# Performance work log

Hardware: AMD Instinct MI355X
Metric: run time of the kernel (lower is better)

## Reference

```python
import jax, jax.numpy as jnp
import numpy as np

N_A = 50000
N_B = 50000
E = 800000
C_IN = 128
C_OUT = 128


def _lstm_cell_seq1(x, W_ih, b):
    # PyTorch LSTM with seq_len=1 and zero initial state: h = o*tanh(i*g)
    # gate order in weight_ih: [i, f, g, o]; f-gate is unused since c0 = 0.
    gates = x @ W_ih.T + b  # [N, 4H]
    i, f, g, o = jnp.split(gates, 4, axis=-1)
    c = jax.nn.sigmoid(i) * jnp.tanh(g)
    return jax.nn.sigmoid(o) * jnp.tanh(c)


def _conv(x_src, x_dst, edge_index, W_ih, b_lstm, W_lin, b_lin):
    # LSTM message depends only on src features -> compute per node, gather per edge.
    msg = _lstm_cell_seq1(x_src, W_ih, b_lstm)          # [N_src, C_OUT]
    src, dst = edge_index[0], edge_index[1]
    aggr = jax.ops.segment_sum(msg[src], dst, num_segments=x_dst.shape[0])  # [N_dst, C_OUT]
    h = jnp.concatenate([x_dst, aggr], axis=-1)          # [N_dst, C_IN + C_OUT]
    return jax.nn.relu(h @ W_lin.T + b_lin)              # dropout = identity (eval mode)


def setup_inputs() -> dict:
    key = jax.random.key(0)
    ks = jax.random.split(key, 12)
    s = 0.05
    return {
        "x_a": jax.random.normal(ks[0], (N_A, C_IN), jnp.float32),
        "x_b": jax.random.normal(ks[1], (N_B, C_IN), jnp.float32),
        "edge_ab": jax.random.randint(ks[2], (2, E), 0, 50000, jnp.int64 if jax.config.jax_enable_x64 else jnp.int32),
        "edge_ba": jax.random.randint(ks[3], (2, E), 0, 50000, jnp.int64 if jax.config.jax_enable_x64 else jnp.int32),
        "W_ih_ab": jax.random.normal(ks[4], (4 * C_OUT, C_IN), jnp.float32) * s,
        "b_ab": jax.random.normal(ks[5], (4 * C_OUT,), jnp.float32) * s,
        "W_lin_ab": jax.random.normal(ks[6], (C_OUT, C_IN + C_OUT), jnp.float32) * s,
        "b_lin_ab": jax.random.normal(ks[7], (C_OUT,), jnp.float32) * s,
        "W_ih_ba": jax.random.normal(ks[8], (4 * C_OUT, C_IN), jnp.float32) * s,
        "b_ba": jax.random.normal(ks[9], (4 * C_OUT,), jnp.float32) * s,
        "W_lin_ba": jax.random.normal(ks[10], (C_OUT, C_IN + C_OUT), jnp.float32) * s,
        "b_lin_ba": jax.random.normal(ks[11], (C_OUT,), jnp.float32) * s,
    }


def reference(x_a, x_b, edge_ab, edge_ba,
              W_ih_ab, b_ab, W_lin_ab, b_lin_ab,
              W_ih_ba, b_ba, W_lin_ba, b_lin_ba):
    # a_to_b relation updates type_b nodes; b_to_a updates type_a nodes.
    out_b = _conv(x_a, x_b, edge_ab, W_ih_ab, b_ab, W_lin_ab, b_lin_ab)
    out_a = _conv(x_b, x_a, edge_ba, W_ih_ba, b_ba, W_lin_ba, b_lin_ba)
    # stack (same shapes) => [2, N, C_OUT]: index 0 = new x_a, index 1 = new x_b
    return jnp.stack([out_a, out_b], axis=0)
```

## Files before the change

kernel.cpp:

```cpp
#include <hip/hip_runtime.h>
#include <cstdint>
#include <cstddef>

#define CCH 128
#define TK 4096
#define FCAP 5120
#define SLOT 5120
#define MAXBKT 512
#define XPAD 136
#define APAD 264

typedef __attribute__((ext_vector_type(8))) short short8;
typedef __attribute__((ext_vector_type(4))) float floatx4;

__device__ __forceinline__ unsigned short f2bf(float f) {
    unsigned u = __builtin_bit_cast(unsigned, f);
    u += 0x7fffu + ((u >> 16) & 1u);
    return (unsigned short)(u >> 16);
}
__device__ __forceinline__ float bf2f(unsigned short h) {
    unsigned u = ((unsigned)h) << 16;
    return __builtin_bit_cast(float, u);
}
__device__ __forceinline__ float sigmoidf_(float x) { return 1.0f / (1.0f + __expf(-x)); }
__device__ __forceinline__ float tanh_fast(float x) {
    x = fminf(fmaxf(x, -10.0f), 10.0f);
    float e = __expf(2.0f * x);
    return (e - 1.0f) / (e + 1.0f);
}

__global__ __launch_bounds__(256) void prep_weights_kernel(
    const float* __restrict__ Wih0, const float* __restrict__ Wih1,
    const float* __restrict__ Wlin0, const float* __restrict__ Wlin1,
    unsigned short* __restrict__ frag_ih, unsigned short* __restrict__ frag_lin)
{
    int t = blockIdx.x * 256 + threadIdx.x;
    if (t < 12288) {
        int l  = t & 63;
        int kc = (t >> 6) & 3;
        int ct = (t >> 8) & 7;
        int g  = (t >> 11) % 3;
        int rel = t / 6144;
        int gb = (g == 0) ? 0 : (g == 1 ? 256 : 384);
        const float* W = rel ? Wih1 : Wih0;
        int n  = gb + ct * 16 + (l & 15);
        int kb = kc * 32 + (l >> 4) * 8;
        unsigned short* o = frag_ih + (size_t)t * 8;
#pragma unroll
        for (int j = 0; j < 8; j++) o[j] = f2bf(W[(size_t)n * CCH + kb + j]);
    } else {
        int t2 = t - 12288;
        if (t2 >= 8192) return;
        int l  = t2 & 63;
        int kc = (t2 >> 6) & 7;
        int ct = (t2 >> 9) & 7;
        int rel = t2 >> 12;
        const float* W = rel ? Wlin1 : Wlin0;
        int n  = ct * 16 + (l & 15);
        int kb = kc * 32 + (l >> 4) * 8;
        unsigned short* o = frag_lin + (size_t)t2 * 8;
#pragma unroll
        for (int j = 0; j < 8; j++) o[j] = f2bf(W[(size_t)n * 256 + kb + j]);
    }
}

__global__ __launch_bounds__(256) void lstm_hist_kernel(
    const float* __restrict__ x0, const float* __restrict__ x1,
    const unsigned short* __restrict__ wfrag,
    const float* __restrict__ b0, const float* __restrict__ b1,
    unsigned short* __restrict__ msg0, unsigned short* __restrict__ msg1,
    int N0, int N1, int nblk0,
    const int* __restrict__ dstE0, const int* __restrict__ dstE1,
    int* __restrict__ H, int E0, int E1, int nbkt0, int NBKT, int nT)
{
    __shared__ unsigned short xs[32 * XPAD];
    __shared__ int h[MAXBKT];
    const int tid = threadIdx.x;

    if (blockIdx.x < nT) {
        for (int i = tid; i < NBKT; i += 256) h[i] = 0;
        __syncthreads();
        const long long Etot = (long long)E0 + E1;
        const long long base = (long long)blockIdx.x * TK;
        for (int i = tid; i < TK; i += 256) {
            long long e = base + i;
            if (e >= Etot) break;
            int g;
            if (e < E0) g = dstE0[e] >> 8;
            else        g = nbkt0 + (dstE1[e - E0] >> 8);
            atomicAdd(&h[g], 1);
        }
        __syncthreads();
        int* row = H + (size_t)blockIdx.x * NBKT;
        for (int i = tid; i < NBKT; i += 256) row[i] = h[i];
        return;
    }

    const int lb = blockIdx.x - nT;
    const int rel = (lb >= nblk0);
    const int nb = (rel ? (lb - nblk0) : lb) * 32;
    const float* x = rel ? x1 : x0;
    const float* bias = rel ? b1 : b0;
    unsigned short* msg = rel ? msg1 : msg0;
    const int N = rel ? N1 : N0;
    const unsigned short* wf = wfrag + (size_t)rel * 6144 * 8;

    {
        int r = tid >> 3;
        int c0 = (tid & 7) * 16;
        int n = nb + r;
        unsigned short* dstp = xs + r * XPAD + c0;
        if (n < N) {
            const float4* srcp = (const float4*)(x + (size_t)n * CCH + c0);
#pragma unroll
            for (int qq = 0; qq < 4; qq++) {
                float4 v = srcp[qq];
                unsigned u0 = (unsigned)f2bf(v.x) | ((unsigned)f2bf(v.y) << 16);
                unsigned u1 = (unsigned)f2bf(v.z) | ((unsigned)f2bf(v.w) << 16);
                *(uint2*)(dstp + qq * 4) = make_uint2(u0, u1);
            }
        } else {
#pragma unroll
            for (int qq = 0; qq < 4; qq++) *(uint2*)(dstp + qq * 4) = make_uint2(0u, 0u);
        }
    }
    __syncthreads();

    const int w = tid >> 6;
    const int l = tid & 63;
    const int ctb2 = w * 2;
    const int q = l >> 4;
    const int m16 = l & 15;

    floatx4 acc[3][2][2];
#pragma unroll
    for (int g = 0; g < 3; g++)
#pragma unroll
        for (int c = 0; c < 2; c++)
#pragma unroll
            for (int mt = 0; mt < 2; mt++) acc[g][c][mt] = (floatx4){0.f, 0.f, 0.f, 0.f};

    const unsigned short* arow0 = xs + m16 * XPAD + q * 8;
    const unsigned short* arow1 = xs + (16 + m16) * XPAD + q * 8;
#pragma unroll
    for (int kc = 0; kc < 4; kc++) {
        short8 af0 = *(const short8*)(arow0 + kc * 32);
        short8 af1 = *(const short8*)(arow1 + kc * 32);
#pragma unroll
        for (int g = 0; g < 3; g++)
#pragma unroll
            for (int c = 0; c < 2; c++) {
                const unsigned short* bp = wf + ((((size_t)g * 8 + (ctb2 + c)) * 4 + kc) * 64 + l) * 8;
                short8 bv = *(const short8*)bp;
                acc[g][c][0] = __builtin_amdgcn_mfma_f32_16x16x32_bf16(af0, bv, acc[g][c][0], 0, 0, 0);
                acc[g][c][1] = __builtin_amdgcn_mfma_f32_16x16x32_bf16(af1, bv, acc[g][c][1], 0, 0, 0);
            }
    }

    __syncthreads();
#pragma unroll
    for (int c = 0; c < 2; c++) {
        const int col = (ctb2 + c) * 16 + m16;
        const float bi = bias[col], bg = bias[256 + col], bo = bias[384 + col];
#pragma unroll
        for (int mt = 0; mt < 2; mt++)
#pragma unroll
            for (int r = 0; r < 4; r++) {
                const int nl = mt * 16 + q * 4 + r;
                float iv = sigmoidf_(acc[0][c][mt][r] + bi);
                float gv = tanh_fast(acc[1][c][mt][r] + bg);
                float ov = sigmoidf_(acc[2][c][mt][r] + bo);
                xs[nl * XPAD + col] = f2bf(ov * tanh_fast(iv * gv));
            }
    }
    __syncthreads();
    {
        int r = tid >> 3;
        int c0 = (tid & 7) * 16;
        int n = nb + r;
        if (n < N) {
            const unsigned short* srow = xs + r * XPAD + c0;
            uint4 v0 = *(const uint4*)(srow);
            uint4 v1 = *(const uint4*)(srow + 8);
            unsigned short* drow = msg + (size_t)n * CCH + c0;
            *(uint4*)(drow) = v0;
            *(uint4*)(drow + 8) = v1;
        }
    }
}

__global__ __launch_bounds__(256) void colscan_kernel(
    int* __restrict__ H, int* __restrict__ btot, int nT, int NBKT)
{
    __shared__ int s[256];
    __shared__ int carry;
    const int g = blockIdx.x;
    const int tid = threadIdx.x;
    if (tid == 0) carry = 0;
    __syncthreads();
    for (int base = 0; base < nT; base += 256) {
        int b = base + tid;
        int v = (b < nT) ? H[(size_t)b * NBKT + g] : 0;
        s[tid] = v;
        __syncthreads();
#pragma unroll
        for (int off = 1; off < 256; off <<= 1) {
            int t = (tid >= off) ? s[tid - off] : 0;
            __syncthreads();
            s[tid] += t;
            __syncthreads();
        }
        if (b < nT) H[(size_t)b * NBKT + g] = s[tid] - v + carry;
        __syncthreads();
        if (tid == 255) carry += s[255];
        __syncthreads();
    }
    if (tid == 0) btot[g] = carry;
}

__global__ __launch_bounds__(256) void tile_scatter_kernel(
    const int* __restrict__ src0, const int* __restrict__ dst0,
    const int* __restrict__ src1, const int* __restrict__ dst1,
    const int* __restrict__ H,
    unsigned* __restrict__ packed, int E0, int E1, int nbkt0, int NBKT)
{
    __shared__ int cur[MAXBKT];
    const int tid = threadIdx.x;
    const int* row = H + (size_t)blockIdx.x * NBKT;
    for (int i = tid; i < NBKT; i += 256) cur[i] = i * SLOT + row[i];
    __syncthreads();
    const long long Etot = (long long)E0 + E1;
    const long long base = (long long)blockIdx.x * TK;
    for (int i = tid; i < TK; i += 256) {
        long long e = base + i;
        if (e >= Etot) break;
        int s, g, k;
        if (e < E0) { int d = dst0[e]; s = src0[e]; g = d >> 8; k = d & 255; }
        else { long long ee = e - E0; int d = dst1[ee]; s = src1[ee]; g = nbkt0 + (d >> 8); k = d & 255; }
        int pos = atomicAdd(&cur[g], 1);
        packed[pos] = ((unsigned)k << 24) | (unsigned)s;
    }
}

__global__ __launch_bounds__(256) void fine_sort_kernel(
    unsigned* __restrict__ packed, const int* __restrict__ btot,
    int* __restrict__ offs0, int* __restrict__ deg0,
    int* __restrict__ offs1, int* __restrict__ deg1,
    int N0, int N1, int nbkt0)
{
    __shared__ unsigned pin[FCAP];
    __shared__ int sout[FCAP];
    __shared__ int hist[256], scn[256], cur[256];
    const int g = blockIdx.x;
    const int tid = threadIdx.x;
    const int base = g * SLOT;
    const int cnt = min(btot[g], FCAP);

    for (int i = tid; i < cnt; i += 256) pin[i] = packed[base + i];
    hist[tid] = 0;
    __syncthreads();
    for (int i = tid; i < cnt; i += 256) atomicAdd(&hist[pin[i] >> 24], 1);
    __syncthreads();
    int v = hist[tid];
    scn[tid] = v;
    __syncthreads();
#pragma unroll
    for (int off = 1; off < 256; off <<= 1) {
        int t = (tid >= off) ? scn[tid - off] : 0;
        __syncthreads();
        scn[tid] += t;
        __syncthreads();
    }
    int excl = scn[tid] - v;
    cur[tid] = excl;
    {
        const int rel = (g >= nbkt0);
        const int lb = rel ? g - nbkt0 : g;
        const int n = lb * 256 + tid;
        const int N = rel ? N1 : N0;
        if (n < N) {
            if (rel) { offs1[n] = base + excl; deg1[n] = v; }
            else     { offs0[n] = base + excl; deg0[n] = v; }
        }
    }
    __syncthreads();
    for (int i = tid; i < cnt; i += 256) {
        unsigned p = pin[i];
        int pos = atomicAdd(&cur[p >> 24], 1);
        sout[pos] = (int)(p & 0x00FFFFFFu);
    }
    __syncthreads();
    int* op = (int*)packed;
    for (int i = tid; i < cnt; i += 256) op[base + i] = sout[i];
}

__global__ __launch_bounds__(512) void gather_linear_kernel(
    const float* __restrict__ xd0, const float* __restrict__ xd1,
    const unsigned short* __restrict__ msg0, const unsigned short* __restrict__ msg1,
    const int* __restrict__ csr,
    const int* __restrict__ offs0, const int* __restrict__ offs1,
    const int* __restrict__ deg0, const int* __restrict__ deg1,
    const unsigned short* __restrict__ wfrag,
    const float* __restrict__ bl0, const float* __restrict__ bl1,
    float* __restrict__ out0, float* __restrict__ out1,
    int P0, int P1, int N0, int N1)
{
    __shared__ unsigned short s[32 * APAD];
    const int tid = threadIdx.x;
    const int grp = blockIdx.x >> 3;
    const int sub = blockIdx.x & 7;
    const int rel = (sub >> 2) & 1;
    const int lb = grp * 4 + (sub & 3);
    const int P = rel ? P1 : P0;
    if (lb >= P) return;
    const int nb = lb * 32;
    const float* xd = rel ? xd1 : xd0;
    const unsigned short* msg = rel ? msg1 : msg0;
    const int* offs = rel ? offs1 : offs0;
    const int* deg = rel ? deg1 : deg0;
    const float* bl = rel ? bl1 : bl0;
    float* outp = rel ? out1 : out0;
    const int N = rel ? N1 : N0;
    const unsigned short* wf = wfrag + (size_t)rel * 4096 * 8;

    {
        int r = tid >> 4;
        int c0 = (tid & 15) * 8;
        int n = nb + r;
        unsigned short* drow = s + r * APAD + c0;
        if (n < N) {
            const float4* srcp = (const float4*)(xd + (size_t)n * CCH + c0);
            float4 v0 = srcp[0], v1 = srcp[1];
            uint4 u;
            u.x = (unsigned)f2bf(v0.x) | ((unsigned)f2bf(v0.y) << 16);
            u.y = (unsigned)f2bf(v0.z) | ((unsigned)f2bf(v0.w) << 16);
            u.z = (unsigned)f2bf(v1.x) | ((unsigned)f2bf(v1.y) << 16);
            u.w = (unsigned)f2bf(v1.z) | ((unsigned)f2bf(v1.w) << 16);
            *(uint4*)drow = u;
        } else {
            *(uint4*)drow = make_uint4(0u, 0u, 0u, 0u);
        }
    }
    {
        const int w = tid >> 6;
        const int l = tid & 63;
        const int g = l >> 4;
        const int c = l & 15;
        const int nloc = w * 4 + g;
        const int n = nb + nloc;
        float a0 = 0.f, a1 = 0.f, a2 = 0.f, a3 = 0.f;
        float a4 = 0.f, a5 = 0.f, a6 = 0.f, a7 = 0.f;
        if (n < N) {
            const int start = offs[n];
            const int cnt = deg[n];
            const int* ce = csr + start;
            const unsigned short* mb = msg + c * 8;
#define ACC8(U) { \
            a0 += bf2f((unsigned short)(U.x)); a1 += bf2f((unsigned short)((U.x) >> 16)); \
            a2 += bf2f((unsigned short)(U.y)); a3 += bf2f((unsigned short)((U.y) >> 16)); \
            a4 += bf2f((unsigned short)(U.z)); a5 += bf2f((unsigned short)((U.z) >> 16)); \
            a6 += bf2f((unsigned short)(U.w)); a7 += bf2f((unsigned short)((U.w) >> 16)); }
            int j = 0;
            for (; j + 4 <= cnt; j += 4) {
                int s0 = ce[j], s1 = ce[j + 1], s2 = ce[j + 2], s3 = ce[j + 3];
                uint4 u0 = *(const uint4*)(mb + (size_t)s0 * CCH);
                uint4 u1 = *(const uint4*)(mb + (size_t)s1 * CCH);
                uint4 u2 = *(const uint4*)(mb + (size_t)s2 * CCH);
                uint4 u3 = *(const uint4*)(mb + (size_t)s3 * CCH);
                ACC8(u0); ACC8(u1); ACC8(u2); ACC8(u3);
            }
            for (; j < cnt; j++) {
                uint4 u0 = *(const uint4*)(mb + (size_t)ce[j] * CCH);
                ACC8(u0);
            }
#undef ACC8
        }
        uint4 o;
        o.x = (unsigned)f2bf(a0) | ((unsigned)f2bf(a1) << 16);
        o.y = (unsigned)f2bf(a2) | ((unsigned)f2bf(a3) << 16);
        o.z = (unsigned)f2bf(a4) | ((unsigned)f2bf(a5) << 16);
        o.w = (unsigned)f2bf(a6) | ((unsigned)f2bf(a7) << 16);
        *(uint4*)(s + nloc * APAD + CCH + c * 8) = o;
    }
    __syncthreads();

    const int w = tid >> 6;
    const int l = tid & 63;
    const int q = l >> 4;
    const int m16 = l & 15;

    floatx4 acc[2];
    acc[0] = (floatx4){0.f, 0.f, 0.f, 0.f};
    acc[1] = (floatx4){0.f, 0.f, 0.f, 0.f};

    const unsigned short* arow0 = s + m16 * APAD + q * 8;
    const unsigned short* arow1 = s + (16 + m16) * APAD + q * 8;
#pragma unroll
    for (int kc = 0; kc < 8; kc++) {
        short8 af0 = *(const short8*)(arow0 + kc * 32);
        short8 af1 = *(const short8*)(arow1 + kc * 32);
        const unsigned short* bp = wf + ((((size_t)w) * 8 + kc) * 64 + l) * 8;
        short8 bv = *(const short8*)bp;
        acc[0] = __builtin_amdgcn_mfma_f32_16x16x32_bf16(af0, bv, acc[0], 0, 0, 0);
        acc[1] = __builtin_amdgcn_mfma_f32_16x16x32_bf16(af1, bv, acc[1], 0, 0, 0);
    }

    const int col = w * 16 + m16;
    const float bv = bl[col];
#pragma unroll
    for (int mt = 0; mt < 2; mt++)
#pragma unroll
        for (int r = 0; r < 4; r++) {
            const int node = nb + mt * 16 + q * 4 + r;
            if (node < N) outp[(size_t)node * CCH + col] = fmaxf(acc[mt][r] + bv, 0.0f);
        }
}

extern "C" void kernel_launch(void* const* d_in, const int* in_sizes, int n_in,
                              void* d_out, int out_size, void* d_ws, size_t ws_size,
                              hipStream_t stream) {
    const float* x_a      = (const float*)d_in[0];
    const float* x_b      = (const float*)d_in[1];
    const int*   e_ab     = (const int*)d_in[2];
    const int*   e_ba     = (const int*)d_in[3];
    const float* W_ih_ab  = (const float*)d_in[4];
    const float* b_ab     = (const float*)d_in[5];
    const float* W_lin_ab = (const float*)d_in[6];
    const float* b_lin_ab = (const float*)d_in[7];
    const float* W_ih_ba  = (const float*)d_in[8];
    const float* b_ba     = (const float*)d_in[9];
    const float* W_lin_ba = (const float*)d_in[10];
    const float* b_lin_ba = (const float*)d_in[11];

    const int NA = in_sizes[0] / CCH;
    const int NB = in_sizes[1] / CCH;
    const int E0 = in_sizes[2] / 2;
    const int E1 = in_sizes[3] / 2;

    float* out = (float*)d_out;
    char* ws = (char*)d_ws;
    size_t off = 0;
    auto alloc = [&](size_t bytes) { char* p = ws + off; off += (bytes + 255) & ~(size_t)255; return p; };

    unsigned short* wfrag_ih  = (unsigned short*)alloc(12288 * 8 * 2);
    unsigned short* wfrag_lin = (unsigned short*)alloc(8192 * 8 * 2);
    unsigned short* msg_a     = (unsigned short*)alloc((size_t)NA * CCH * 2);
    unsigned short* msg_b     = (unsigned short*)alloc((size_t)NB * CCH * 2);

    const int nbkt0 = (NB + 255) / 256;
    const int nbkt1 = (NA + 255) / 256;
    const int NBKT = nbkt0 + nbkt1;
    const long long Etot = (long long)E0 + E1;
    const int nT = (int)((Etot + TK - 1) / TK);

    int* H      = (int*)alloc((size_t)nT * NBKT * 4);
    int* btot   = (int*)alloc((size_t)NBKT * 4);
    int* offs_b = (int*)alloc((size_t)NB * 4);
    int* offs_a = (int*)alloc((size_t)NA * 4);
    int* deg_b  = (int*)alloc((size_t)NB * 4);
    int* deg_a  = (int*)alloc((size_t)NA * 4);
    unsigned* packed = (unsigned*)alloc((size_t)NBKT * SLOT * 4);

    const int nblkA = (NA + 31) / 32;
    const int nblkB = (NB + 31) / 32;

    prep_weights_kernel<<<80, 256, 0, stream>>>(
        W_ih_ab, W_ih_ba, W_lin_ab, W_lin_ba, wfrag_ih, wfrag_lin);

    lstm_hist_kernel<<<nT + nblkA + nblkB, 256, 0, stream>>>(
        x_a, x_b, wfrag_ih, b_ab, b_ba, msg_a, msg_b, NA, NB, nblkA,
        e_ab + E0, e_ba + E1, H, E0, E1, nbkt0, NBKT, nT);

    colscan_kernel<<<NBKT, 256, 0, stream>>>(H, btot, nT, NBKT);
    tile_scatter_kernel<<<nT, 256, 0, stream>>>(
        e_ab, e_ab + E0, e_ba, e_ba + E1, H, packed, E0, E1, nbkt0, NBKT);
    fine_sort_kernel<<<NBKT, 256, 0, stream>>>(
        packed, btot, offs_b, deg_b, offs_a, deg_a, NB, NA, nbkt0);

    const int Pmax = (nblkB > nblkA) ? nblkB : nblkA;
    const int G = ((Pmax + 3) / 4) * 8;
    gather_linear_kernel<<<G, 512, 0, stream>>>(
        x_b, x_a, msg_a, msg_b, (const int*)packed,
        offs_b, offs_a, deg_b, deg_a, wfrag_lin, b_lin_ab, b_lin_ba,
        out + (size_t)NA * CCH, out, nblkB, nblkA, NB, NA);
}
```

Baseline: 263.7 us.

## Replace two-level bucket sort with global-atomic degree count and direct scatter

Replaces the tile histogram, column scan, tile scatter and in-bucket fine sort with per-node global atomic degree counting, a per-256-node bucket prefix scan, and a direct scatter using per-node global atomic cursors. The degree arrays are zeroed inside the weight-prep kernel. This removes one kernel launch, the large histogram matrix and the shared-memory fine sort. In exchange it issues about 1.6M global atomics on random addresses twice, and the order of edges within each destination becomes nondeterministic.

```diff
diff --git a/kernel.cpp b/kernel.cpp
--- a/kernel.cpp
+++ b/kernel.cpp
@@ -4,9 +4,7 @@
 
 #define CCH 128
 #define TK 4096
-#define FCAP 5120
 #define SLOT 5120
-#define MAXBKT 512
 #define XPAD 136
 #define APAD 264
 
@@ -32,7 +30,8 @@
 __global__ __launch_bounds__(256) void prep_weights_kernel(
     const float* __restrict__ Wih0, const float* __restrict__ Wih1,
     const float* __restrict__ Wlin0, const float* __restrict__ Wlin1,
-    unsigned short* __restrict__ frag_ih, unsigned short* __restrict__ frag_lin)
+    unsigned short* __restrict__ frag_ih, unsigned short* __restrict__ frag_lin,
+    int* __restrict__ degB, int* __restrict__ degA, int NBn, int NAn)
 {
     int t = blockIdx.x * 256 + threadIdx.x;
     if (t < 12288) {
@@ -48,9 +47,8 @@
         unsigned short* o = frag_ih + (size_t)t * 8;
 #pragma unroll
         for (int j = 0; j < 8; j++) o[j] = f2bf(W[(size_t)n * CCH + kb + j]);
-    } else {
+    } else if (t < 20480) {
         int t2 = t - 12288;
-        if (t2 >= 8192) return;
         int l  = t2 & 63;
         int kc = (t2 >> 6) & 7;
         int ct = (t2 >> 9) & 7;
@@ -61,38 +59,35 @@
         unsigned short* o = frag_lin + (size_t)t2 * 8;
 #pragma unroll
         for (int j = 0; j < 8; j++) o[j] = f2bf(W[(size_t)n * 256 + kb + j]);
-    }
-}
-
-__global__ __launch_bounds__(256) void lstm_hist_kernel(
+    } else {
+        int z = t - 20480;
+        if (z < NBn) degB[z] = 0;
+        else if (z - NBn < NAn) degA[z - NBn] = 0;
+    }
+}
+
+__global__ __launch_bounds__(256) void lstm_deg_kernel(
     const float* __restrict__ x0, const float* __restrict__ x1,
     const unsigned short* __restrict__ wfrag,
     const float* __restrict__ b0, const float* __restrict__ b1,
     unsigned short* __restrict__ msg0, unsigned short* __restrict__ msg1,
     int N0, int N1, int nblk0,
     const int* __restrict__ dstE0, const int* __restrict__ dstE1,
-    int* __restrict__ H, int E0, int E1, int nbkt0, int NBKT, int nT)
+    int* __restrict__ degB, int* __restrict__ degA,
+    int E0, int E1, int nT)
 {
     __shared__ unsigned short xs[32 * XPAD];
-    __shared__ int h[MAXBKT];
     const int tid = threadIdx.x;
 
     if (blockIdx.x < nT) {
-        for (int i = tid; i < NBKT; i += 256) h[i] = 0;
-        __syncthreads();
         const long long Etot = (long long)E0 + E1;
         const long long base = (long long)blockIdx.x * TK;
         for (int i = tid; i < TK; i += 256) {
             long long e = base + i;
             if (e >= Etot) break;
-            int g;
-            if (e < E0) g = dstE0[e] >> 8;
-            else        g = nbkt0 + (dstE1[e - E0] >> 8);
-            atomicAdd(&h[g], 1);
-        }
-        __syncthreads();
-        int* row = H + (size_t)blockIdx.x * NBKT;
-        for (int i = tid; i < NBKT; i += 256) row[i] = h[i];
+            if (e < E0) atomicAdd(&degB[dstE0[e]], 1);
+            else        atomicAdd(&degA[dstE1[e - E0]], 1);
+        }
         return;
     }
 
@@ -189,109 +184,55 @@
     }
 }
 
-__global__ __launch_bounds__(256) void colscan_kernel(
-    int* __restrict__ H, int* __restrict__ btot, int nT, int NBKT)
+__global__ __launch_bounds__(256) void bucket_scan_kernel(
+    const int* __restrict__ degB, const int* __restrict__ degA,
+    int* __restrict__ offsB, int* __restrict__ offsA,
+    int* __restrict__ curB, int* __restrict__ curA,
+    int NBn, int NAn, int nbkt0)
 {
     __shared__ int s[256];
-    __shared__ int carry;
     const int g = blockIdx.x;
     const int tid = threadIdx.x;
-    if (tid == 0) carry = 0;
+    const int rel = (g >= nbkt0);
+    const int lb = rel ? g - nbkt0 : g;
+    const int n = lb * 256 + tid;
+    const int N = rel ? NAn : NBn;
+    const int* deg = rel ? degA : degB;
+    int v = (n < N) ? deg[n] : 0;
+    s[tid] = v;
     __syncthreads();
-    for (int base = 0; base < nT; base += 256) {
-        int b = base + tid;
-        int v = (b < nT) ? H[(size_t)b * NBKT + g] : 0;
-        s[tid] = v;
+#pragma unroll
+    for (int off = 1; off < 256; off <<= 1) {
+        int t = (tid >= off) ? s[tid - off] : 0;
         __syncthreads();
-#pragma unroll
-        for (int off = 1; off < 256; off <<= 1) {
-            int t = (tid >= off) ? s[tid - off] : 0;
-            __syncthreads();
-            s[tid] += t;
-            __syncthreads();
-        }
-        if (b < nT) H[(size_t)b * NBKT + g] = s[tid] - v + carry;
+        s[tid] += t;
         __syncthreads();
-        if (tid == 255) carry += s[255];
-        __syncthreads();
-    }
-    if (tid == 0) btot[g] = carry;
-}
-
-__global__ __launch_bounds__(256) void tile_scatter_kernel(
+    }
+    if (n < N) {
+        int o = g * SLOT + (s[tid] - v);
+        if (rel) { offsA[n] = o; curA[n] = o; }
+        else     { offsB[n] = o; curB[n] = o; }
+    }
+}
+
+__global__ __launch_bounds__(256) void scatter_kernel(
     const int* __restrict__ src0, const int* __restrict__ dst0,
     const int* __restrict__ src1, const int* __restrict__ dst1,
-    const int* __restrict__ H,
-    unsigned* __restrict__ packed, int E0, int E1, int nbkt0, int NBKT)
+    int* __restrict__ curB, int* __restrict__ curA,
+    int* __restrict__ csr, int E0, int E1, int csrMax)
 {
-    __shared__ int cur[MAXBKT];
     const int tid = threadIdx.x;
-    const int* row = H + (size_t)blockIdx.x * NBKT;
-    for (int i = tid; i < NBKT; i += 256) cur[i] = i * SLOT + row[i];
-    __syncthreads();
     const long long Etot = (long long)E0 + E1;
     const long long base = (long long)blockIdx.x * TK;
     for (int i = tid; i < TK; i += 256) {
         long long e = base + i;
         if (e >= Etot) break;
-        int s, g, k;
-        if (e < E0) { int d = dst0[e]; s = src0[e]; g = d >> 8; k = d & 255; }
-        else { long long ee = e - E0; int d = dst1[ee]; s = src1[ee]; g = nbkt0 + (d >> 8); k = d & 255; }
-        int pos = atomicAdd(&cur[g], 1);
-        packed[pos] = ((unsigned)k << 24) | (unsigned)s;
-    }
-}
-
-__global__ __launch_bounds__(256) void fine_sort_kernel(
-    unsigned* __restrict__ packed, const int* __restrict__ btot,
-    int* __restrict__ offs0, int* __restrict__ deg0,
-    int* __restrict__ offs1, int* __restrict__ deg1,
-    int N0, int N1, int nbkt0)
-{
-    __shared__ unsigned pin[FCAP];
-    __shared__ int sout[FCAP];
-    __shared__ int hist[256], scn[256], cur[256];
-    const int g = blockIdx.x;
-    const int tid = threadIdx.x;
-    const int base = g * SLOT;
-    const int cnt = min(btot[g], FCAP);
-
-    for (int i = tid; i < cnt; i += 256) pin[i] = packed[base + i];
-    hist[tid] = 0;
-    __syncthreads();
-    for (int i = tid; i < cnt; i += 256) atomicAdd(&hist[pin[i] >> 24], 1);
-    __syncthreads();
-    int v = hist[tid];
-    scn[tid] = v;
-    __syncthreads();
-#pragma unroll
-    for (int off = 1; off < 256; off <<= 1) {
-        int t = (tid >= off) ? scn[tid - off] : 0;
-        __syncthreads();
-        scn[tid] += t;
-        __syncthreads();
-    }
-    int excl = scn[tid] - v;
-    cur[tid] = excl;
-    {
-        const int rel = (g >= nbkt0);
-        const int lb = rel ? g - nbkt0 : g;
-        const int n = lb * 256 + tid;
-        const int N = rel ? N1 : N0;
-        if (n < N) {
-            if (rel) { offs1[n] = base + excl; deg1[n] = v; }
-            else     { offs0[n] = base + excl; deg0[n] = v; }
-        }
-    }
-    __syncthreads();
-    for (int i = tid; i < cnt; i += 256) {
-        unsigned p = pin[i];
-        int pos = atomicAdd(&cur[p >> 24], 1);
-        sout[pos] = (int)(p & 0x00FFFFFFu);
-    }
-    __syncthreads();
-    int* op = (int*)packed;
-    for (int i = tid; i < cnt; i += 256) op[base + i] = sout[i];
+        int s, pos;
+        if (e < E0) { s = src0[e]; pos = atomicAdd(&curB[dst0[e]], 1); }
+        else { long long ee = e - E0; s = src1[ee]; pos = atomicAdd(&curA[dst1[ee]], 1); }
+        pos = min(pos, csrMax);
+        csr[pos] = s;
+    }
 }
 
 __global__ __launch_bounds__(512) void gather_linear_kernel(
@@ -453,34 +394,37 @@
     const long long Etot = (long long)E0 + E1;
     const int nT = (int)((Etot + TK - 1) / TK);
 
-    int* H      = (int*)alloc((size_t)nT * NBKT * 4);
-    int* btot   = (int*)alloc((size_t)NBKT * 4);
+    int* cur_b  = (int*)alloc((size_t)NB * 4);
+    int* cur_a  = (int*)alloc((size_t)NA * 4);
     int* offs_b = (int*)alloc((size_t)NB * 4);
     int* offs_a = (int*)alloc((size_t)NA * 4);
     int* deg_b  = (int*)alloc((size_t)NB * 4);
     int* deg_a  = (int*)alloc((size_t)NA * 4);
-    unsigned* packed = (unsigned*)alloc((size_t)NBKT * SLOT * 4);
+    int* csr    = (int*)alloc((size_t)NBKT * SLOT * 4);
 
     const int nblkA = (NA + 31) / 32;
     const int nblkB = (NB + 31) / 32;
 
-    prep_weights_kernel<<<80, 256, 0, stream>>>(
-        W_ih_ab, W_ih_ba, W_lin_ab, W_lin_ba, wfrag_ih, wfrag_lin);
-
-    lstm_hist_kernel<<<nT + nblkA + nblkB, 256, 0, stream>>>(
+    const int prepG = 80 + (NA + NB + 255) / 256;
+    prep_weights_kernel<<<prepG, 256, 0, stream>>>(
+        W_ih_ab, W_ih_ba, W_lin_ab, W_lin_ba, wfrag_ih, wfrag_lin,
+        deg_b, deg_a, NB, NA);
+
+    lstm_deg_kernel<<<nT + nblkA + nblkB, 256, 0, stream>>>(
         x_a, x_b, wfrag_ih, b_ab, b_ba, msg_a, msg_b, NA, NB, nblkA,
-        e_ab + E0, e_ba + E1, H, E0, E1, nbkt0, NBKT, nT);
-
-    colscan_kernel<<<NBKT, 256, 0, stream>>>(H, btot, nT, NBKT);
-    tile_scatter_kernel<<<nT, 256, 0, stream>>>(
-        e_ab, e_ab + E0, e_ba, e_ba + E1, H, packed, E0, E1, nbkt0, NBKT);
-    fine_sort_kernel<<<NBKT, 256, 0, stream>>>(
-        packed, btot, offs_b, deg_b, offs_a, deg_a, NB, NA, nbkt0);
+        e_ab + E0, e_ba + E1, deg_b, deg_a, E0, E1, nT);
+
+    bucket_scan_kernel<<<NBKT, 256, 0, stream>>>(
+        deg_b, deg_a, offs_b, offs_a, cur_b, cur_a, NB, NA, nbkt0);
+
+    scatter_kernel<<<nT, 256, 0, stream>>>(
+        e_ab, e_ab + E0, e_ba, e_ba + E1, cur_b, cur_a, csr, E0, E1,
+        NBKT * SLOT - 1);
 
     const int Pmax = (nblkB > nblkA) ? nblkB : nblkA;
     const int G = ((Pmax + 3) / 4) * 8;
     gather_linear_kernel<<<G, 512, 0, stream>>>(
-        x_b, x_a, msg_a, msg_b, (const int*)packed,
+        x_b, x_a, msg_a, msg_b, csr,
         offs_b, offs_a, deg_b, deg_a, wfrag_lin, b_lin_ab, b_lin_ba,
         out + (size_t)NA * CCH, out, nblkB, nblkA, NB, NA);
 }
```

Result: slower. 395.9 us (+50.1%).
